# Performance work log

Hardware: AMD Instinct MI355X
Metric: run time of the kernel (lower is better)

Reference implementation:

```python
import jax, jax.numpy as jnp
import numpy as np

DIM = 1024
N_HEADS = 16
HEAD_DIM = DIM // N_HEADS
LN_EPS = 1e-5


def layer_norm(x, gamma, beta, eps=LN_EPS):
    mu = jnp.mean(x, axis=-1, keepdims=True)
    var = jnp.var(x, axis=-1, keepdims=True)
    return (x - mu) * jax.lax.rsqrt(var + eps) * gamma + beta


def setup_inputs() -> dict:
    key = jax.random.key(0)
    ks = jax.random.split(key, 12)
    B, Nq, Nc, D = 2, 1024, 4096, DIM
    s = 1.0 / np.sqrt(D)  # torch Linear default init scale (uniform bound)
    inp = {
        "query": jax.random.normal(ks[0], (B, Nq, D), jnp.float32),
        "context": jax.random.normal(ks[1], (B, Nc, D), jnp.float32),
        "wq": jax.random.uniform(ks[2], (D, D), jnp.float32, -s, s),
        "bq": jax.random.uniform(ks[3], (D,), jnp.float32, -s, s),
        "wk": jax.random.uniform(ks[4], (D, D), jnp.float32, -s, s),
        "bk": jax.random.uniform(ks[5], (D,), jnp.float32, -s, s),
        "wv": jax.random.uniform(ks[6], (D, D), jnp.float32, -s, s),
        "bv": jax.random.uniform(ks[7], (D,), jnp.float32, -s, s),
        "wo": jax.random.uniform(ks[8], (D, D), jnp.float32, -s, s),
        "bo": jax.random.uniform(ks[9], (D,), jnp.float32, -s, s),
        "g_q": jnp.ones((D,), jnp.float32),
        "b_q": jnp.zeros((D,), jnp.float32),
        "g_kv": jnp.ones((D,), jnp.float32),
        "b_kv": jnp.zeros((D,), jnp.float32),
    }
    return inp


def reference(query, context, wq, bq, wk, bk, wv, bv, wo, bo, g_q, b_q, g_kv, b_kv):
    B, Nq, D = query.shape
    Nc = context.shape[1]
    H, Hd = N_HEADS, HEAD_DIM

    qn = layer_norm(query, g_q, b_q)        # [B,Nq,D]
    cn = layer_norm(context, g_kv, b_kv)    # [B,Nc,D]

    # torch Linear: y = x @ W.T + b; weights here stored as [out,in]
    Q = (jnp.einsum('bnd,ed->bne', qn, wq) + bq).reshape(B, Nq, H, Hd)
    K = (jnp.einsum('bnd,ed->bne', cn, wk) + bk).reshape(B, Nc, H, Hd)
    V = (jnp.einsum('bnd,ed->bne', cn, wv) + bv).reshape(B, Nc, H, Hd)

    scale = 1.0 / np.sqrt(Hd)
    scores = jnp.einsum('bqhd,bkhd->bhqk', Q, K) * scale  # [B,H,Nq,Nc]
    attn = jax.nn.softmax(scores, axis=-1)
    out = jnp.einsum('bhqk,bkhd->bqhd', attn, V).reshape(B, Nq, D)

    return qn + (jnp.einsum('bnd,ed->bne', out, wo) + bo)
```

## Files before the change

### kernel.cpp

```cpp
#include <hip/hip_runtime.h>

typedef unsigned short u16;
typedef __attribute__((ext_vector_type(8))) __bf16 bf16x8;
typedef __attribute__((ext_vector_type(4))) float f32x4;

struct alignas(8) U16x4 { u16 x, y, z, w; };

#define MFMA16(a, b, c) __builtin_amdgcn_mfma_f32_16x16x32_bf16(a, b, c, 0, 0, 0)

__device__ __forceinline__ u16 f2bf(float f) {
    union { float f; unsigned u; } v; v.f = f;
    unsigned r = v.u + 0x7fffu + ((v.u >> 16) & 1u);
    return (u16)(r >> 16);
}

__device__ __forceinline__ float bf2f(u16 b) {
    union { unsigned u; float f; } v; v.u = (unsigned)b << 16;
    return v.f;
}

__device__ __forceinline__ unsigned cvt_pk_bf16(float lo, float hi) {
    unsigned r;
    asm("v_cvt_pk_bf16_f32 %0, %1, %2" : "=v"(r) : "v"(lo), "v"(hi));
    return r;
}

__device__ __forceinline__ float fexp2(float x) {
    float r;
    asm("v_exp_f32 %0, %1" : "=v"(r) : "v"(x));
    return r;
}

__device__ __forceinline__ void gload_lds16(const void* g, void* l) {
    __builtin_amdgcn_global_load_lds(
        (__attribute__((address_space(1))) void*)g,
        (__attribute__((address_space(3))) void*)l, 16, 0, 0);
}

__global__ __launch_bounds__(256)
void prep(const float* __restrict__ query, const float* __restrict__ context,
          const float* __restrict__ g_q, const float* __restrict__ b_q,
          const float* __restrict__ g_kv, const float* __restrict__ b_kv,
          u16* __restrict__ qnb, u16* __restrict__ cnb,
          const float4* __restrict__ w0, const float4* __restrict__ w1,
          const float4* __restrict__ w2, const float4* __restrict__ w3,
          U16x4* __restrict__ o0, U16x4* __restrict__ o1,
          U16x4* __restrict__ o2, U16x4* __restrict__ o3)
{
    const int blk = blockIdx.x;
    if (blk < 2560) {
        const float *x, *g, *be; u16* y16; int rb;
        if (blk < 512) { x = query;   g = g_q;  be = b_q;  y16 = qnb; rb = blk; }
        else           { x = context; g = g_kv; be = b_kv; y16 = cnb; rb = blk - 512; }
        const int wid = threadIdx.x >> 6, lane = threadIdx.x & 63;
        const size_t row = (size_t)rb * 4 + wid;
        const float4* xr = (const float4*)(x + row * 1024);
        float4 v[4];
        float s = 0.f, ss = 0.f;
#pragma unroll
        for (int i = 0; i < 4; ++i) {
            v[i] = xr[i * 64 + lane];
            s  += (v[i].x + v[i].y) + (v[i].z + v[i].w);
            ss += (v[i].x * v[i].x + v[i].y * v[i].y) + (v[i].z * v[i].z + v[i].w * v[i].w);
        }
#pragma unroll
        for (int o = 32; o; o >>= 1) { s += __shfl_xor(s, o, 64); ss += __shfl_xor(ss, o, 64); }
        const float mu = s * (1.f / 1024.f);
        const float rstd = rsqrtf(ss * (1.f / 1024.f) - mu * mu + 1e-5f);
#pragma unroll
        for (int i = 0; i < 4; ++i) {
            float4 gv = ((const float4*)g)[i * 64 + lane];
            float4 bv = ((const float4*)be)[i * 64 + lane];
            float4 o;
            o.x = (v[i].x - mu) * rstd * gv.x + bv.x;
            o.y = (v[i].y - mu) * rstd * gv.y + bv.y;
            o.z = (v[i].z - mu) * rstd * gv.z + bv.z;
            o.w = (v[i].w - mu) * rstd * gv.w + bv.w;
            U16x4 pk = { f2bf(o.x), f2bf(o.y), f2bf(o.z), f2bf(o.w) };
            ((U16x4*)(y16 + row * 1024))[i * 64 + lane] = pk;
        }
    } else {
        const int i = (blk - 2560) * 256 + threadIdx.x;
        float4 v;
        v = w0[i]; o0[i] = { f2bf(v.x), f2bf(v.y), f2bf(v.z), f2bf(v.w) };
        v = w1[i]; o1[i] = { f2bf(v.x), f2bf(v.y), f2bf(v.z), f2bf(v.w) };
        v = w2[i]; o2[i] = { f2bf(v.x), f2bf(v.y), f2bf(v.z), f2bf(v.w) };
        v = w3[i]; o3[i] = { f2bf(v.x), f2bf(v.y), f2bf(v.z), f2bf(v.w) };
    }
}

__global__ __launch_bounds__(512, 2)
void gemm_kv8(const u16* __restrict__ A, const u16* __restrict__ Wkv,
              const float* __restrict__ bkp, const float* __restrict__ bvp,
              u16* __restrict__ Kout, u16* __restrict__ Vt)
{
    __shared__ __align__(16) u16 smem[65536];

    const int tid = threadIdx.x, wid = tid >> 6, lane = tid & 63;
    const int lr = lane & 15, lg = lane >> 4;
    const int rs = lr & 7;
    const int wm = wid >> 2, wn = wid & 3;

    const int fid = blockIdx.x;
    const int wk = (fid & 7) * 32 + (fid >> 3);
    const int nt = wk >> 5, mt = wk & 31;
    const int row0 = mt * 256, col0 = nt * 256;

    const int sr = tid >> 3;
    const int sc = tid & 7;
    const int scol = (sc ^ (sr & 7)) * 8;

    auto stA = [&](int buf, int h, int ko) {
#pragma unroll
        for (int i = 0; i < 2; ++i)
            gload_lds16(A + (size_t)(row0 + h * 128 + i * 64 + sr) * 1024 + ko + scol,
                        (char*)smem + buf * 32768 + h * 16384 + i * 8192 + wid * 1024);
    };
    auto stB = [&](int buf, int s, int ko) {
        gload_lds16(Wkv + (size_t)(col0 + (tid >> 7) * 64 + s * 16 + ((tid >> 3) & 15)) * 1024 + ko + scol,
                    (char*)smem + 65536 + buf * 32768 + s * 8192 + wid * 1024);
    };

    f32x4 acc[8][4];
#pragma unroll
    for (int m = 0; m < 8; ++m)
#pragma unroll
        for (int n = 0; n < 4; ++n) acc[m][n] = (f32x4){0.f, 0.f, 0.f, 0.f};

    stA(0, 0, 0);  stA(0, 1, 0);
    stB(0, 0, 0);  stB(0, 1, 0);  stB(0, 2, 0);  stB(0, 3, 0);
    stA(1, 0, 64); stA(1, 1, 64);
    stB(1, 0, 64); stB(1, 1, 64); stB(1, 2, 64);
    asm volatile("s_waitcnt vmcnt(7)" ::: "memory");
    __builtin_amdgcn_s_barrier();

    for (int kt = 0; kt < 16; ++kt) {
        const int cur = kt & 1;
        const int ko1 = (kt < 15 ? kt + 1 : 15) * 64;
        const int ko2 = (kt < 14 ? kt + 2 : 15) * 64;
        const u16* Ab = &smem[cur * 16384 + wm * 8192];
        const u16* Bb = &smem[32768 + cur * 16384 + wn * 1024];

        bf16x8 af[8][2];
#pragma unroll
        for (int m = 0; m < 8; ++m)
#pragma unroll
            for (int kk = 0; kk < 2; ++kk)
                af[m][kk] = *(const bf16x8*)&Ab[(m * 16 + lr) * 64 + ((kk * 4 + lg) ^ rs) * 8];
        {
            bf16x8 b0 = *(const bf16x8*)&Bb[0 * 4096 + lr * 64 + (lg ^ rs) * 8];
            bf16x8 b1 = *(const bf16x8*)&Bb[0 * 4096 + lr * 64 + ((4 + lg) ^ rs) * 8];
            stB(cur ^ 1, 3, ko1);
            __builtin_amdgcn_s_setprio(1);
#pragma unroll
            for (int m = 0; m < 8; ++m) acc[m][0] = MFMA16(af[m][0], b0, acc[m][0]);
#pragma unroll
            for (int m = 0; m < 8; ++m) acc[m][0] = MFMA16(af[m][1], b1, acc[m][0]);
            __builtin_amdgcn_s_setprio(0);
        }
        __builtin_amdgcn_s_barrier();

        {
            bf16x8 b0 = *(const bf16x8*)&Bb[1 * 4096 + lr * 64 + (lg ^ rs) * 8];
            bf16x8 b1 = *(const bf16x8*)&Bb[1 * 4096 + lr * 64 + ((4 + lg) ^ rs) * 8];
            stA(cur, 0, ko2);
            stB(cur, 0, ko2);
            __builtin_amdgcn_s_setprio(1);
#pragma unroll
            for (int m = 0; m < 8; ++m) acc[m][1] = MFMA16(af[m][0], b0, acc[m][1]);
#pragma unroll
            for (int m = 0; m < 8; ++m) acc[m][1] = MFMA16(af[m][1], b1, acc[m][1]);
            __builtin_amdgcn_s_setprio(0);
        }
        asm volatile("s_waitcnt vmcnt(12)" ::: "memory");
        __builtin_amdgcn_s_barrier();

        {
            bf16x8 b0 = *(const bf16x8*)&Bb[2 * 4096 + lr * 64 + (lg ^ rs) * 8];
            bf16x8 b1 = *(const bf16x8*)&Bb[2 * 4096 + lr * 64 + ((4 + lg) ^ rs) * 8];
            stA(cur, 1, ko2);
            stB(cur, 1, ko2);
            __builtin_amdgcn_s_setprio(1);
#pragma unroll
            for (int m = 0; m < 8; ++m) acc[m][2] = MFMA16(af[m][0], b0, acc[m][2]);
#pragma unroll
            for (int m = 0; m < 8; ++m) acc[m][2] = MFMA16(af[m][1], b1, acc[m][2]);
            __builtin_amdgcn_s_setprio(0);
        }
        asm volatile("s_waitcnt vmcnt(14)" ::: "memory");
        __builtin_amdgcn_s_barrier();

        {
            bf16x8 b0 = *(const bf16x8*)&Bb[3 * 4096 + lr * 64 + (lg ^ rs) * 8];
            bf16x8 b1 = *(const bf16x8*)&Bb[3 * 4096 + lr * 64 + ((4 + lg) ^ rs) * 8];
            stB(cur, 2, ko2);
            __builtin_amdgcn_s_setprio(1);
#pragma unroll
            for (int m = 0; m < 8; ++m) acc[m][3] = MFMA16(af[m][0], b0, acc[m][3]);
#pragma unroll
            for (int m = 0; m < 8; ++m) acc[m][3] = MFMA16(af[m][1], b1, acc[m][3]);
            __builtin_amdgcn_s_setprio(0);
        }
        asm volatile("s_waitcnt vmcnt(9)" ::: "memory");
        __builtin_amdgcn_s_barrier();
    }
    asm volatile("s_waitcnt vmcnt(0)" ::: "memory");

    const bool is_v = (nt >= 4);
#pragma unroll
    for (int m = 0; m < 8; ++m) {
#pragma unroll
        for (int n = 0; n < 4; ++n) {
            const int r = row0 + wm * 128 + m * 16 + lg * 4;
            const int ncol = col0 + wn * 64 + n * 16 + lr;
            if (!is_v) {
                const float kb = bkp[ncol];
#pragma unroll
                for (int j = 0; j < 4; ++j)
                    Kout[(size_t)(r + j) * 1024 + ncol] = f2bf(acc[m][n][j] + kb);
            } else {
                const int vc = ncol - 1024;
                const float vb = bvp[vc];
                const size_t base = ((size_t)(r >> 12) * 1024 + vc) * 4096 + (r & 4095);
                U16x4 pk = { f2bf(acc[m][n][0] + vb), f2bf(acc[m][n][1] + vb),
                             f2bf(acc[m][n][2] + vb), f2bf(acc[m][n][3] + vb) };
                *(U16x4*)&Vt[base] = pk;
            }
        }
    }
}

template<int MODE>
__global__ __launch_bounds__(256)
void gemm_bt64(const u16* __restrict__ A, const u16* __restrict__ W,
               const float* __restrict__ bias, const u16* __restrict__ resid,
               void* __restrict__ Cp, int M, int N, int K, float alpha)
{
    constexpr int BK = 64;
    __shared__ __align__(16) u16 sA[64 * BK];
    __shared__ __align__(16) u16 sB[128 * BK];
    const int tid = threadIdx.x, wid = tid >> 6, lane = tid & 63;
    const int lr = lane & 15, lg = lane >> 4;
    const int wr = wid >> 1, wc = wid & 1;
    const int row0 = blockIdx.x * 64, col0 = blockIdx.y * 128;
    const int srow = wid * 8 + (lane >> 3), scol = (lane & 7) * 8;

    const u16* Ag = A + (size_t)(row0 + srow) * K + scol;
    const u16* Wg = W + (size_t)(col0 + srow) * K + scol;

    f32x4 acc[2][4];
#pragma unroll
    for (int m = 0; m < 2; ++m)
#pragma unroll
        for (int n = 0; n < 4; ++n) acc[m][n] = (f32x4){0.f, 0.f, 0.f, 0.f};

    for (int k0 = 0; k0 < K; k0 += BK) {
        __syncthreads();
#pragma unroll
        for (int i = 0; i < 2; ++i)
            gload_lds16(Ag + (size_t)i * 32 * K + k0, (char*)sA + i * 4096 + wid * 1024);
#pragma unroll
        for (int i = 0; i < 4; ++i)
            gload_lds16(Wg + (size_t)i * 32 * K + k0, (char*)sB + i * 4096 + wid * 1024);
        __syncthreads();
#pragma unroll
        for (int kk = 0; kk < 2; ++kk) {
            bf16x8 af[2], bfr[4];
#pragma unroll
            for (int m = 0; m < 2; ++m)
                af[m] = *(const bf16x8*)&sA[(wr * 32 + m * 16 + lr) * BK + kk * 32 + lg * 8];
#pragma unroll
            for (int n = 0; n < 4; ++n)
                bfr[n] = *(const bf16x8*)&sB[(wc * 64 + n * 16 + lr) * BK + kk * 32 + lg * 8];
#pragma unroll
            for (int m = 0; m < 2; ++m)
#pragma unroll
                for (int n = 0; n < 4; ++n)
                    acc[m][n] = MFMA16(af[m], bfr[n], acc[m][n]);
        }
    }

#pragma unroll
    for (int m = 0; m < 2; ++m) {
#pragma unroll
        for (int n = 0; n < 4; ++n) {
            const int r = row0 + wr * 32 + m * 16 + lg * 4;
            const int c = col0 + wc * 64 + n * 16 + lr;
            const float bv = bias[c];
            if constexpr (MODE == 0) {
                u16* C = (u16*)Cp;
#pragma unroll
                for (int j = 0; j < 4; ++j)
                    C[(size_t)(r + j) * N + c] = f2bf((acc[m][n][j] + bv) * alpha);
            } else {
                float* C = (float*)Cp;
#pragma unroll
                for (int j = 0; j < 4; ++j)
                    C[(size_t)(r + j) * N + c] =
                        (acc[m][n][j] + bv) + bf2f(resid[(size_t)(r + j) * N + c]);
            }
        }
    }
}

__global__ __launch_bounds__(512, 4)
void attn_fwd(const u16* __restrict__ Q, const u16* __restrict__ Kg,
              const u16* __restrict__ Vt, u16* __restrict__ O)
{
    constexpr int D = 1024, CSTR = 19;
    __shared__ __align__(16) char smem[81920];

    const int tid = threadIdx.x, wid = tid >> 6, lane = tid & 63;
    const int grp = wid >> 2, w = wid & 3;
    const int lr = lane & 15, lg = lane >> 4;
    const int rs = lr & 7;
    const int pkey = (lr & 7) << 4;

    const int fid = blockIdx.x;
    const int wk = (fid & 7) * 64 + (fid >> 3);
    const int qblk = wk & 15, h = (wk >> 4) & 15, b = wk >> 8;
    const int q0 = qblk * 64 + w * 16;

    const u16* Qrow = Q + (size_t)(b * 1024 + q0 + lr) * D + h * 64;
    const bf16x8 qf0 = *(const bf16x8*)(Qrow + lg * 8);
    const bf16x8 qf1 = *(const bf16x8*)(Qrow + 32 + lg * 8);

    const int srow = w * 8 + (lane >> 3);
    const int scol = ((lane & 7) ^ (srow & 7)) * 8;
    const u16* kp = Kg + (size_t)(b * 4096 + grp * 2048 + srow) * D + h * 64 + scol;
    const u16* vp = Vt + ((size_t)(b * 16 + h) * 64 + srow) * 4096 + grp * 2048 + scol;

    char* sProw = smem + 65536 + wid * 2048 + lr * 128;

    f32x4 po[4];
#pragma unroll
    for (int df = 0; df < 4; ++df) po[df] = (f32x4){0.f, 0.f, 0.f, 0.f};
    float m = -INFINITY, l = 0.f;

    {
        char* kd = smem + grp * 8192 + w * 1024;
        char* vd = smem + 32768 + grp * 8192 + w * 1024;
        gload_lds16(kp,                      kd);
        gload_lds16(kp + (size_t)32 * D,     kd + 4096);
        gload_lds16(vp,                      vd);
        gload_lds16(vp + (size_t)32 * 4096,  vd + 4096);
        kp += (size_t)64 * D; vp += 64;
    }
    asm volatile("s_waitcnt vmcnt(0)" ::: "memory");
    asm volatile("s_barrier" ::: "memory");

    for (int t = 0; t < 32; ++t) {
        const int cur = t & 1;
        if (t < 31) {
            char* kd = smem + (cur ^ 1) * 16384 + grp * 8192 + w * 1024;
            char* vd = smem + 32768 + (cur ^ 1) * 16384 + grp * 8192 + w * 1024;
            gload_lds16(kp,                      kd);
            gload_lds16(kp + (size_t)32 * D,     kd + 4096);
            gload_lds16(vp,                      vd);
            gload_lds16(vp + (size_t)32 * 4096,  vd + 4096);
            kp += (size_t)64 * D; vp += 64;
        }

        const u16* kb = (const u16*)(smem + cur * 16384 + grp * 8192);
        const u16* vb = (const u16*)(smem + 32768 + cur * 16384 + grp * 8192);

        f32x4 s4[4];
#pragma unroll
        for (int f = 0; f < 4; ++f) {
            const int r = f * 16 + lr;
            bf16x8 k0v = *(const bf16x8*)&kb[r * 64 + (lg ^ rs) * 8];
            bf16x8 k1v = *(const bf16x8*)&kb[r * 64 + ((lg + 4) ^ rs) * 8];
            f32x4 z = (f32x4){0.f, 0.f, 0.f, 0.f};
            z = MFMA16(k0v, qf0, z);
            s4[f] = MFMA16(k1v, qf1, z);
        }

        float pmax = fmaxf(fmaxf(fmaxf(s4[0][0], s4[0][1]), fmaxf(s4[0][2], s4[0][3])),
                     fmaxf(fmaxf(fmaxf(s4[1][0], s4[1][1]), fmaxf(s4[1][2], s4[1][3])),
                     fmaxf(fmaxf(fmaxf(s4[2][0], s4[2][1]), fmaxf(s4[2][2], s4[2][3])),
                           fmaxf(fmaxf(s4[3][0], s4[3][1]), fmaxf(s4[3][2], s4[3][3])))));
        if (!__all(pmax <= m)) {
            float tmax = fmaxf(pmax, __shfl_xor(pmax, 16, 64));
            tmax = fmaxf(tmax, __shfl_xor(tmax, 32, 64));
            const float mn = fmaxf(m, tmax);
            const float corr = fexp2(m - mn);
            l *= corr;
#pragma unroll
            for (int df = 0; df < 4; ++df) po[df] *= corr;
            m = mn;
        }
        float lsum = 0.f;
        uint2 pk[4];
#pragma unroll
        for (int f = 0; f < 4; ++f) {
            float p0 = fexp2(s4[f][0] - m);
            float p1 = fexp2(s4[f][1] - m);
            float p2 = fexp2(s4[f][2] - m);
            float p3 = fexp2(s4[f][3] - m);
            lsum += (p0 + p1) + (p2 + p3);
            pk[f].x = cvt_pk_bf16(p0, p1);
            pk[f].y = cvt_pk_bf16(p2, p3);
        }
        l += lsum;

#pragma unroll
        for (int f = 0; f < 4; ++f)
            *(uint2*)(sProw + ((f * 32 + lg * 8) ^ pkey)) = pk[f];

#pragma unroll
        for (int c = 0; c < 2; ++c) {
            bf16x8 pf = *(const bf16x8*)(sProw + ((c * 64 + lg * 16) ^ pkey));
#pragma unroll
            for (int df = 0; df < 4; ++df) {
                const int r = df * 16 + lr;
                bf16x8 vf = *(const bf16x8*)&vb[r * 64 + ((c * 4 + lg) ^ rs) * 8];
                po[df] = MFMA16(vf, pf, po[df]);
            }
        }

        asm volatile("s_waitcnt vmcnt(0)" ::: "memory");
        asm volatile("s_barrier" ::: "memory");
    }

    l += __shfl_xor(l, 16, 64);
    l += __shfl_xor(l, 32, 64);

    float* cb = (float*)smem;
    if (grp == 1) {
        float* dst = cb + (size_t)(w * 64 + lane) * CSTR;
        dst[0] = m; dst[1] = l;
#pragma unroll
        for (int df = 0; df < 4; ++df)
#pragma unroll
            for (int j = 0; j < 4; ++j) dst[2 + df * 4 + j] = po[df][j];
    }
    __syncthreads();
    if (grp == 0) {
        const float* src = cb + (size_t)(w * 64 + lane) * CSTR;
        const float m1 = src[0], l1 = src[1];
        const float M = fmaxf(m, m1);
        const float c0 = fexp2(m - M), c1 = fexp2(m1 - M);
        const float rl = 1.f / (l * c0 + l1 * c1);
        u16* Orow = O + (size_t)(b * 1024 + q0 + lr) * D + h * 64;
#pragma unroll
        for (int df = 0; df < 4; ++df) {
            U16x4 opk = { f2bf((po[df][0] * c0 + src[2 + df * 4 + 0] * c1) * rl),
                          f2bf((po[df][1] * c0 + src[2 + df * 4 + 1] * c1) * rl),
                          f2bf((po[df][2] * c0 + src[2 + df * 4 + 2] * c1) * rl),
                          f2bf((po[df][3] * c0 + src[2 + df * 4 + 3] * c1) * rl) };
            *(U16x4*)&Orow[df * 16 + lg * 4] = opk;
        }
    }
}

extern "C" void kernel_launch(void* const* d_in, const int* in_sizes, int n_in,
                              void* d_out, int out_size, void* d_ws, size_t ws_size,
                              hipStream_t stream)
{
    const float* query   = (const float*)d_in[0];
    const float* context = (const float*)d_in[1];
    const float* wq = (const float*)d_in[2];
    const float* bq = (const float*)d_in[3];
    const float* wk = (const float*)d_in[4];
    const float* bk = (const float*)d_in[5];
    const float* wv = (const float*)d_in[6];
    const float* bv = (const float*)d_in[7];
    const float* wo = (const float*)d_in[8];
    const float* bo = (const float*)d_in[9];
    const float* g_q  = (const float*)d_in[10];
    const float* b_q  = (const float*)d_in[11];
    const float* g_kv = (const float*)d_in[12];
    const float* b_kv = (const float*)d_in[13];

    char* p = (char*)d_ws;
    auto alloc = [&](size_t bytes) { char* r = p; p += (bytes + 255) & ~(size_t)255; return r; };
    u16*   wqb  = (u16*)alloc(1024 * 1024 * 2);
    u16*   wkb  = (u16*)alloc(1024 * 1024 * 2);
    u16*   wvb  = (u16*)alloc(1024 * 1024 * 2);
    u16*   wob  = (u16*)alloc(1024 * 1024 * 2);
    u16*   qnb  = (u16*)alloc((size_t)2048 * 1024 * 2);
    u16*   cnb  = (u16*)alloc((size_t)8192 * 1024 * 2);
    u16*   Qb   = (u16*)alloc((size_t)2048 * 1024 * 2);
    u16*   Kb   = (u16*)alloc((size_t)8192 * 1024 * 2);
    u16*   Vtb  = (u16*)alloc((size_t)8192 * 1024 * 2);
    u16*   AOb  = (u16*)alloc((size_t)2048 * 1024 * 2);

    prep<<<3584, 256, 0, stream>>>(query, context, g_q, b_q, g_kv, b_kv,
                                   qnb, cnb,
                                   (const float4*)wq, (const float4*)wk,
                                   (const float4*)wv, (const float4*)wo,
                                   (U16x4*)wqb, (U16x4*)wkb, (U16x4*)wvb, (U16x4*)wob);

    gemm_bt64<0><<<dim3(32, 8), 256, 0, stream>>>(qnb, wqb, bq, nullptr, Qb, 2048, 1024, 1024, 0.18033688f);
    gemm_kv8<<<dim3(256), 512, 0, stream>>>(cnb, wkb, bk, bv, Kb, Vtb);

    attn_fwd<<<dim3(512), 512, 0, stream>>>(Qb, Kb, Vtb, AOb);

    gemm_bt64<1><<<dim3(32, 8), 256, 0, stream>>>(AOb, wob, bo, qnb, d_out, 2048, 1024, 1024, 1.0f);
}
```

Baseline: 161.4 us.

## Use 32x32 MFMA in attention with in-register P transpose via permlane32_swap

Rewrites the attention kernel so each wave owns 32 query rows and uses 32x32x16 bf16 MFMA for both QK^T and PV, with four waves per block instead of eight. The probability tile is converted to the B-operand layout in registers using permlane32_swap, which removes the LDS round trip for P and its extra barrier-free stores and loads. The goal is fewer LDS operations and higher MFMA efficiency per instruction. In exchange each wave holds more accumulator registers, there are fewer waves to hide latency, and the new lane mapping has to be exactly right.

```diff
diff --git a/kernel.cpp b/kernel.cpp
--- a/kernel.cpp
+++ b/kernel.cpp
@@ -3,10 +3,13 @@
 typedef unsigned short u16;
 typedef __attribute__((ext_vector_type(8))) __bf16 bf16x8;
 typedef __attribute__((ext_vector_type(4))) float f32x4;
+typedef __attribute__((ext_vector_type(16))) float f32x16;
+typedef __attribute__((ext_vector_type(2))) int i32x2;
 
 struct alignas(8) U16x4 { u16 x, y, z, w; };
 
 #define MFMA16(a, b, c) __builtin_amdgcn_mfma_f32_16x16x32_bf16(a, b, c, 0, 0, 0)
+#define MFMA32(a, b, c) __builtin_amdgcn_mfma_f32_32x32x16_bf16(a, b, c, 0, 0, 0)
 
 __device__ __forceinline__ u16 f2bf(float f) {
     union { float f; unsigned u; } v; v.f = f;
@@ -303,126 +306,133 @@
     }
 }
 
-__global__ __launch_bounds__(512, 4)
+__global__ __launch_bounds__(256, 2)
 void attn_fwd(const u16* __restrict__ Q, const u16* __restrict__ Kg,
               const u16* __restrict__ Vt, u16* __restrict__ O)
 {
-    constexpr int D = 1024, CSTR = 19;
-    __shared__ __align__(16) char smem[81920];
+    constexpr int D = 1024, CSTR = 35;
+    __shared__ __align__(16) char smem[65536];
 
     const int tid = threadIdx.x, wid = tid >> 6, lane = tid & 63;
-    const int grp = wid >> 2, w = wid & 3;
-    const int lr = lane & 15, lg = lane >> 4;
-    const int rs = lr & 7;
-    const int pkey = (lr & 7) << 4;
+    const int grp = wid >> 1, w = wid & 1;
+    const int q32 = lane & 31, hf = lane >> 5;
+    const int rk = lane & 7;
 
     const int fid = blockIdx.x;
     const int wk = (fid & 7) * 64 + (fid >> 3);
-    const int qblk = wk & 15, h = (wk >> 4) & 15, b = wk >> 8;
-    const int q0 = qblk * 64 + w * 16;
-
-    const u16* Qrow = Q + (size_t)(b * 1024 + q0 + lr) * D + h * 64;
-    const bf16x8 qf0 = *(const bf16x8*)(Qrow + lg * 8);
-    const bf16x8 qf1 = *(const bf16x8*)(Qrow + 32 + lg * 8);
-
-    const int srow = w * 8 + (lane >> 3);
-    const int scol = ((lane & 7) ^ (srow & 7)) * 8;
-    const u16* kp = Kg + (size_t)(b * 4096 + grp * 2048 + srow) * D + h * 64 + scol;
-    const u16* vp = Vt + ((size_t)(b * 16 + h) * 64 + srow) * 4096 + grp * 2048 + scol;
-
-    char* sProw = smem + 65536 + wid * 2048 + lr * 128;
-
-    f32x4 po[4];
-#pragma unroll
-    for (int df = 0; df < 4; ++df) po[df] = (f32x4){0.f, 0.f, 0.f, 0.f};
+    const int qblk = wk & 15, head = (wk >> 4) & 15, b = wk >> 8;
+    const int q0 = qblk * 64 + w * 32;
+
+    const u16* Qrow = Q + (size_t)(b * 1024 + q0 + q32) * D + head * 64;
+    bf16x8 qf[4];
+#pragma unroll
+    for (int ds = 0; ds < 4; ++ds)
+        qf[ds] = *(const bf16x8*)(Qrow + ds * 16 + hf * 8);
+
+    const int sr3 = lane >> 3;
+    const int scol = ((lane & 7) ^ (sr3 & 7)) * 8;
+    const u16* kp = Kg + (size_t)(b * 4096 + grp * 2048 + w * 32 + sr3) * D + head * 64 + scol;
+    const u16* vp = Vt + ((size_t)(b * 16 + head) * 64 + w * 32 + sr3) * 4096 + grp * 2048 + scol;
+
+    auto stage = [&](int buf, int kv0) {
+        char* kd = smem + buf * 16384 + grp * 8192 + w * 4096;
+        char* vd = smem + 32768 + buf * 16384 + grp * 8192 + w * 4096;
+#pragma unroll
+        for (int c = 0; c < 4; ++c) {
+            gload_lds16(kp + (size_t)(kv0 + c * 8) * D,     kd + c * 1024);
+            gload_lds16(vp + (size_t)(c * 8) * 4096 + kv0,  vd + c * 1024);
+        }
+    };
+
+    f32x16 o0, o1;
+#pragma unroll
+    for (int r = 0; r < 16; ++r) { o0[r] = 0.f; o1[r] = 0.f; }
     float m = -INFINITY, l = 0.f;
 
-    {
-        char* kd = smem + grp * 8192 + w * 1024;
-        char* vd = smem + 32768 + grp * 8192 + w * 1024;
-        gload_lds16(kp,                      kd);
-        gload_lds16(kp + (size_t)32 * D,     kd + 4096);
-        gload_lds16(vp,                      vd);
-        gload_lds16(vp + (size_t)32 * 4096,  vd + 4096);
-        kp += (size_t)64 * D; vp += 64;
-    }
+    stage(0, 0);
     asm volatile("s_waitcnt vmcnt(0)" ::: "memory");
     asm volatile("s_barrier" ::: "memory");
 
     for (int t = 0; t < 32; ++t) {
         const int cur = t & 1;
-        if (t < 31) {
-            char* kd = smem + (cur ^ 1) * 16384 + grp * 8192 + w * 1024;
-            char* vd = smem + 32768 + (cur ^ 1) * 16384 + grp * 8192 + w * 1024;
-            gload_lds16(kp,                      kd);
-            gload_lds16(kp + (size_t)32 * D,     kd + 4096);
-            gload_lds16(vp,                      vd);
-            gload_lds16(vp + (size_t)32 * 4096,  vd + 4096);
-            kp += (size_t)64 * D; vp += 64;
-        }
+        if (t < 31) stage(cur ^ 1, (t + 1) * 64);
 
         const u16* kb = (const u16*)(smem + cur * 16384 + grp * 8192);
         const u16* vb = (const u16*)(smem + 32768 + cur * 16384 + grp * 8192);
 
-        f32x4 s4[4];
-#pragma unroll
-        for (int f = 0; f < 4; ++f) {
-            const int r = f * 16 + lr;
-            bf16x8 k0v = *(const bf16x8*)&kb[r * 64 + (lg ^ rs) * 8];
-            bf16x8 k1v = *(const bf16x8*)&kb[r * 64 + ((lg + 4) ^ rs) * 8];
-            f32x4 z = (f32x4){0.f, 0.f, 0.f, 0.f};
-            z = MFMA16(k0v, qf0, z);
-            s4[f] = MFMA16(k1v, qf1, z);
-        }
-
-        float pmax = fmaxf(fmaxf(fmaxf(s4[0][0], s4[0][1]), fmaxf(s4[0][2], s4[0][3])),
-                     fmaxf(fmaxf(fmaxf(s4[1][0], s4[1][1]), fmaxf(s4[1][2], s4[1][3])),
-                     fmaxf(fmaxf(fmaxf(s4[2][0], s4[2][1]), fmaxf(s4[2][2], s4[2][3])),
-                           fmaxf(fmaxf(s4[3][0], s4[3][1]), fmaxf(s4[3][2], s4[3][3])))));
+        f32x16 s0, s1;
+#pragma unroll
+        for (int r = 0; r < 16; ++r) { s0[r] = 0.f; s1[r] = 0.f; }
+#pragma unroll
+        for (int ds = 0; ds < 4; ++ds) {
+            bf16x8 kf0 = *(const bf16x8*)&kb[(q32) * 64      + ((ds * 2 + hf) ^ rk) * 8];
+            bf16x8 kf1 = *(const bf16x8*)&kb[(32 + q32) * 64 + ((ds * 2 + hf) ^ rk) * 8];
+            s0 = MFMA32(kf0, qf[ds], s0);
+            s1 = MFMA32(kf1, qf[ds], s1);
+        }
+
+        float pmax = s0[0];
+#pragma unroll
+        for (int r = 1; r < 16; ++r) pmax = fmaxf(pmax, s0[r]);
+#pragma unroll
+        for (int r = 0; r < 16; ++r) pmax = fmaxf(pmax, s1[r]);
+        pmax = fmaxf(pmax, __shfl_xor(pmax, 32, 64));
         if (!__all(pmax <= m)) {
-            float tmax = fmaxf(pmax, __shfl_xor(pmax, 16, 64));
-            tmax = fmaxf(tmax, __shfl_xor(tmax, 32, 64));
-            const float mn = fmaxf(m, tmax);
+            const float mn = fmaxf(m, pmax);
             const float corr = fexp2(m - mn);
             l *= corr;
 #pragma unroll
-            for (int df = 0; df < 4; ++df) po[df] *= corr;
+            for (int r = 0; r < 16; ++r) { o0[r] *= corr; o1[r] *= corr; }
             m = mn;
         }
         float lsum = 0.f;
-        uint2 pk[4];
-#pragma unroll
-        for (int f = 0; f < 4; ++f) {
-            float p0 = fexp2(s4[f][0] - m);
-            float p1 = fexp2(s4[f][1] - m);
-            float p2 = fexp2(s4[f][2] - m);
-            float p3 = fexp2(s4[f][3] - m);
-            lsum += (p0 + p1) + (p2 + p3);
-            pk[f].x = cvt_pk_bf16(p0, p1);
-            pk[f].y = cvt_pk_bf16(p2, p3);
-        }
+#pragma unroll
+        for (int r = 0; r < 16; ++r) { s0[r] = fexp2(s0[r] - m); lsum += s0[r]; }
+#pragma unroll
+        for (int r = 0; r < 16; ++r) { s1[r] = fexp2(s1[r] - m); lsum += s1[r]; }
         l += lsum;
 
-#pragma unroll
-        for (int f = 0; f < 4; ++f)
-            *(uint2*)(sProw + ((f * 32 + lg * 8) ^ pkey)) = pk[f];
-
-#pragma unroll
-        for (int c = 0; c < 2; ++c) {
-            bf16x8 pf = *(const bf16x8*)(sProw + ((c * 64 + lg * 16) ^ pkey));
-#pragma unroll
-            for (int df = 0; df < 4; ++df) {
-                const int r = df * 16 + lr;
-                bf16x8 vf = *(const bf16x8*)&vb[r * 64 + ((c * 4 + lg) ^ rs) * 8];
-                po[df] = MFMA16(vf, pf, po[df]);
+        bf16x8 pa[4];
+#pragma unroll
+        for (int mt = 0; mt < 2; ++mt) {
+#pragma unroll
+            for (int kq = 0; kq < 2; ++kq) {
+                const int s_ = 8 * kq;
+                float e0, e1, e2, e3, e4, e5, e6, e7;
+                if (mt == 0) {
+                    e0 = s0[s_+0]; e1 = s0[s_+1]; e2 = s0[s_+2]; e3 = s0[s_+3];
+                    e4 = s0[s_+4]; e5 = s0[s_+5]; e6 = s0[s_+6]; e7 = s0[s_+7];
+                } else {
+                    e0 = s1[s_+0]; e1 = s1[s_+1]; e2 = s1[s_+2]; e3 = s1[s_+3];
+                    e4 = s1[s_+4]; e5 = s1[s_+5]; e6 = s1[s_+6]; e7 = s1[s_+7];
+                }
+                unsigned wa = cvt_pk_bf16(e0, e1);
+                unsigned wb = cvt_pk_bf16(e4, e5);
+                unsigned wc = cvt_pk_bf16(e2, e3);
+                unsigned wd = cvt_pk_bf16(e6, e7);
+                i32x2 r02 = __builtin_amdgcn_permlane32_swap((int)wa, (int)wb, false, false);
+                i32x2 r13 = __builtin_amdgcn_permlane32_swap((int)wc, (int)wd, false, false);
+                union { unsigned u[4]; bf16x8 v; } uw;
+                uw.u[0] = (unsigned)r02[0];
+                uw.u[1] = (unsigned)r13[0];
+                uw.u[2] = (unsigned)r02[1];
+                uw.u[3] = (unsigned)r13[1];
+                pa[mt * 2 + kq] = uw.v;
             }
+        }
+
+#pragma unroll
+        for (int ks = 0; ks < 4; ++ks) {
+            bf16x8 vf0 = *(const bf16x8*)&vb[(q32) * 64      + ((ks * 2 + hf) ^ rk) * 8];
+            bf16x8 vf1 = *(const bf16x8*)&vb[(32 + q32) * 64 + ((ks * 2 + hf) ^ rk) * 8];
+            o0 = MFMA32(vf0, pa[ks], o0);
+            o1 = MFMA32(vf1, pa[ks], o1);
         }
 
         asm volatile("s_waitcnt vmcnt(0)" ::: "memory");
         asm volatile("s_barrier" ::: "memory");
     }
 
-    l += __shfl_xor(l, 16, 64);
     l += __shfl_xor(l, 32, 64);
 
     float* cb = (float*)smem;
@@ -430,9 +440,7 @@
         float* dst = cb + (size_t)(w * 64 + lane) * CSTR;
         dst[0] = m; dst[1] = l;
 #pragma unroll
-        for (int df = 0; df < 4; ++df)
-#pragma unroll
-            for (int j = 0; j < 4; ++j) dst[2 + df * 4 + j] = po[df][j];
+        for (int r = 0; r < 16; ++r) { dst[2 + r] = o0[r]; dst[18 + r] = o1[r]; }
     }
     __syncthreads();
     if (grp == 0) {
@@ -441,14 +449,26 @@
         const float M = fmaxf(m, m1);
         const float c0 = fexp2(m - M), c1 = fexp2(m1 - M);
         const float rl = 1.f / (l * c0 + l1 * c1);
-        u16* Orow = O + (size_t)(b * 1024 + q0 + lr) * D + h * 64;
-#pragma unroll
-        for (int df = 0; df < 4; ++df) {
-            U16x4 opk = { f2bf((po[df][0] * c0 + src[2 + df * 4 + 0] * c1) * rl),
-                          f2bf((po[df][1] * c0 + src[2 + df * 4 + 1] * c1) * rl),
-                          f2bf((po[df][2] * c0 + src[2 + df * 4 + 2] * c1) * rl),
-                          f2bf((po[df][3] * c0 + src[2 + df * 4 + 3] * c1) * rl) };
-            *(U16x4*)&Orow[df * 16 + lg * 4] = opk;
+        u16* Orow = O + (size_t)(b * 1024 + q0 + q32) * D + head * 64;
+#pragma unroll
+        for (int dt = 0; dt < 2; ++dt) {
+#pragma unroll
+            for (int rq = 0; rq < 4; ++rq) {
+                float v0, v1, v2, v3;
+                if (dt == 0) {
+                    v0 = (o0[rq*4+0] * c0 + src[2 + rq*4+0] * c1) * rl;
+                    v1 = (o0[rq*4+1] * c0 + src[2 + rq*4+1] * c1) * rl;
+                    v2 = (o0[rq*4+2] * c0 + src[2 + rq*4+2] * c1) * rl;
+                    v3 = (o0[rq*4+3] * c0 + src[2 + rq*4+3] * c1) * rl;
+                } else {
+                    v0 = (o1[rq*4+0] * c0 + src[18 + rq*4+0] * c1) * rl;
+                    v1 = (o1[rq*4+1] * c0 + src[18 + rq*4+1] * c1) * rl;
+                    v2 = (o1[rq*4+2] * c0 + src[18 + rq*4+2] * c1) * rl;
+                    v3 = (o1[rq*4+3] * c0 + src[18 + rq*4+3] * c1) * rl;
+                }
+                U16x4 pk = { f2bf(v0), f2bf(v1), f2bf(v2), f2bf(v3) };
+                *(U16x4*)&Orow[dt * 32 + rq * 8 + hf * 4] = pk;
+            }
         }
     }
 }
@@ -494,7 +514,7 @@
     gemm_bt64<0><<<dim3(32, 8), 256, 0, stream>>>(qnb, wqb, bq, nullptr, Qb, 2048, 1024, 1024, 0.18033688f);
     gemm_kv8<<<dim3(256), 512, 0, stream>>>(cnb, wkb, bk, bv, Kb, Vtb);
 
-    attn_fwd<<<dim3(512), 512, 0, stream>>>(Qb, Kb, Vtb, AOb);
+    attn_fwd<<<dim3(512), 256, 0, stream>>>(Qb, Kb, Vtb, AOb);
 
     gemm_bt64<1><<<dim3(32, 8), 256, 0, stream>>>(AOb, wob, bo, qnb, d_out, 2048, 1024, 1024, 1.0f);
 }
```

New measurement: 155.8 us. 1.04x faster.
